# Kernel optimization log

Hardware: AMD Instinct MI355X
Metric: run time of the kernel (lower is better)

## Reference

```python
import jax, jax.numpy as jnp
import numpy as np

NUM_LEVELS = 4
RADIUS = 4


def _avg_pool2(x):
    # x: [N, H, W] -> [N, H//2, W//2], 2x2 mean pool, stride 2 (F.avg_pool2d(corr,2,2))
    N, H, W = x.shape
    return x.reshape(N, H // 2, 2, W // 2, 2).mean(axis=(2, 4))


def _bilinear_sample(img, x, y):
    # img: [N, H, W]; x, y: [N, P] pixel coords.
    # Matches F.grid_sample(..., mode='bilinear', align_corners=True, padding_mode='zeros')
    # after the pixel->normalized->pixel round trip in bilinear_sampler (identity).
    N, H, W = img.shape
    x0 = jnp.floor(x)
    y0 = jnp.floor(y)
    wx = x - x0
    wy = y - y0
    x0i = x0.astype(jnp.int32)
    y0i = y0.astype(jnp.int32)
    flat = img.reshape(N, H * W)

    def gather(yi, xi):
        valid = (xi >= 0) & (xi <= W - 1) & (yi >= 0) & (yi <= H - 1)
        idx = jnp.clip(yi, 0, H - 1) * W + jnp.clip(xi, 0, W - 1)
        v = jnp.take_along_axis(flat, idx, axis=1)
        return jnp.where(valid, v, jnp.zeros((), img.dtype))

    v00 = gather(y0i, x0i)
    v01 = gather(y0i, x0i + 1)
    v10 = gather(y0i + 1, x0i)
    v11 = gather(y0i + 1, x0i + 1)
    return (v00 * (1 - wy) * (1 - wx) + v01 * (1 - wy) * wx
            + v10 * wy * (1 - wx) + v11 * wy * wx)


def _corr_block(fmap1, fmap2, coords):
    B, D, H, W = fmap1.shape
    # all-pairs correlation: [B, H*W, H*W] / sqrt(D)
    f1 = fmap1.reshape(B, D, H * W)
    f2 = fmap2.reshape(B, D, H * W)
    corr = jnp.einsum('bdn,bdm->bnm', f1, f2) / jnp.sqrt(jnp.asarray(D, fmap1.dtype))
    corr = corr.reshape(B * H * W, H, W)
    pyramid = [corr]
    for _ in range(NUM_LEVELS - 1):
        corr = _avg_pool2(corr)
        pyramid.append(corr)

    # coords: [B, 2, H, W] (x, y) -> [B*H*W, 2]
    c = coords.transpose(0, 2, 3, 1).reshape(B * H * W, 2)
    r = RADIUS
    d = jnp.linspace(-r, r, 2 * r + 1)
    dyg, dxg = jnp.meshgrid(d, d, indexing='ij')
    # faithful to torch: delta = stack(meshgrid(dy, dx), -1); channel 0 added to x, 1 to y
    delta = jnp.stack([dyg, dxg], axis=-1).reshape(-1, 2)  # [81, 2]

    outs = []
    for i, lvl in enumerate(pyramid):
        cl = c[:, None, :] / (2.0 ** i) + delta[None, :, :]  # [N, 81, 2]
        s = _bilinear_sample(lvl, cl[..., 0], cl[..., 1])    # [N, 81]
        outs.append(s.reshape(B, H, W, (2 * r + 1) ** 2))
    out = jnp.concatenate(outs, axis=-1)                     # [B, H, W, 4*81]
    return out.transpose(0, 3, 1, 2).astype(jnp.float32)


def setup_inputs() -> dict:
    key = jax.random.key(0)
    k1, k2, k3 = jax.random.split(key, 3)
    B, D, H, W = 2, 256, 80, 80
    fmap1 = jax.random.normal(k1, (B, D, H, W), dtype=jnp.float32)
    fmap2 = jax.random.normal(k2, (B, D, H, W), dtype=jnp.float32)
    # pixel coords in [0, W-1] x [0, H-1] (channel 0 = x, channel 1 = y)
    u = jax.random.uniform(k3, (B, 2, H, W), dtype=jnp.float32)
    scale = jnp.asarray([W - 1, H - 1], jnp.float32).reshape(1, 2, 1, 1)
    coords = u * scale
    return {"fmap1": fmap1, "fmap2": fmap2, "coords": coords}


def reference(fmap1, fmap2, coords):
    return _corr_block(fmap1, fmap2, coords)
```

## Files before the change

kernel.cpp:

```cpp
#include <hip/hip_runtime.h>


typedef _Float16 h2 __attribute__((ext_vector_type(2)));
typedef _Float16 half8 __attribute__((ext_vector_type(8)));
typedef float f32x4 __attribute__((ext_vector_type(4)));

#define HWDIM 80
#define DCH 256
#define NPIX 12800
#define NBUCKET 800

__global__ __launch_bounds__(256) void transpose_all(const float* __restrict__ f1,
                                                     const float* __restrict__ f2,
                                                     _Float16* __restrict__ f1h,
                                                     _Float16* __restrict__ f2p0) {
    __shared__ float tile[256][33];
    int bid = blockIdx.x;
    bool isf1 = bid < 400;
    int lb = isf1 ? bid : bid - 400;
    const float* src = isf1 ? f1 : f2;
    int b = lb / 200;
    int s0 = (lb % 200) * 32;
    int t = threadIdx.x;
    const float* sb = src + (size_t)b * DCH * (HWDIM * HWDIM);
#pragma unroll 4
    for (int k = 0; k < 32; ++k) {
        int j = t + 256 * k;
        int c = j >> 5, s = j & 31;
        tile[c][s] = sb[(size_t)c * (HWDIM * HWDIM) + s0 + s];
    }
    __syncthreads();
    int p = t & 127;
    int srow = t >> 7;
    if (isf1) {
        _Float16* db = f1h + ((size_t)b * 6400 + s0) * DCH;
#pragma unroll 4
        for (int k = 0; k < 16; ++k) {
            int s = 2 * k + srow;
            h2 v;
            v[0] = (_Float16)tile[2 * p][s];
            v[1] = (_Float16)tile[2 * p + 1][s];
            *(h2*)(db + (size_t)s * DCH + 2 * p) = v;
        }
    } else {
#pragma unroll 4
        for (int k = 0; k < 16; ++k) {
            int s = 2 * k + srow;
            int spatial = s0 + s;
            int yy = spatial / 80;
            int xx = spatial - yy * 80;
            h2 v;
            v[0] = (_Float16)tile[2 * p][s];
            v[1] = (_Float16)tile[2 * p + 1][s];
            size_t off = (size_t)b * 2073600 + (size_t)(p >> 4) * 259200
                       + ((size_t)(yy + 5) * 90 + (xx + 5)) * 32 + ((2 * p) & 31);
            *(h2*)(f2p0 + off) = v;
        }
    }
}

__global__ __launch_bounds__(256) void pool1(const _Float16* __restrict__ src,
                                             _Float16* __restrict__ dst) {
    int i = blockIdx.x * 256 + threadIdx.x;
    int c2 = i & 15;
    int r = i >> 4;
    int x = r % 40; r /= 40;
    int y = r % 40; r /= 40;
    int pl = r & 7;
    int b = r >> 3;
    const h2* s = (const h2*)src + ((size_t)b * 2073600 + (size_t)pl * 259200) / 2
                + ((size_t)(2 * y + 5) * 90 + (2 * x + 5)) * 16 + c2;
    h2 v00 = s[0], v01 = s[16], v10 = s[90 * 16], v11 = s[90 * 16 + 16];
    float r0 = ((float)v00[0] + (float)v01[0] + (float)v10[0] + (float)v11[0]) * 0.25f;
    float r1 = ((float)v00[1] + (float)v01[1] + (float)v10[1] + (float)v11[1]) * 0.25f;
    h2 o; o[0] = (_Float16)r0; o[1] = (_Float16)r1;
    *((h2*)dst + ((size_t)b * 640000 + (size_t)pl * 80000) / 2
      + ((size_t)(y + 5) * 50 + (x + 5)) * 16 + c2) = o;
}

__global__ __launch_bounds__(256) void pool23(const _Float16* __restrict__ l1,
                                              _Float16* __restrict__ l2,
                                              _Float16* __restrict__ l3) {
    int i = blockIdx.x * 256 + threadIdx.x;
    if (i < 102400) {
        int c2 = i & 15;
        int r = i >> 4;
        int x = r % 20; r /= 20;
        int y = r % 20; r /= 20;
        int pl = r & 7;
        int b = r >> 3;
        const h2* s = (const h2*)l1 + ((size_t)b * 640000 + (size_t)pl * 80000) / 2
                    + ((size_t)(2 * y + 5) * 50 + (2 * x + 5)) * 16 + c2;
        h2 v00 = s[0], v01 = s[16], v10 = s[50 * 16], v11 = s[50 * 16 + 16];
        float r0 = ((float)v00[0] + (float)v01[0] + (float)v10[0] + (float)v11[0]) * 0.25f;
        float r1 = ((float)v00[1] + (float)v01[1] + (float)v10[1] + (float)v11[1]) * 0.25f;
        h2 o; o[0] = (_Float16)r0; o[1] = (_Float16)r1;
        *((h2*)l2 + ((size_t)b * 230400 + (size_t)pl * 28800) / 2
          + ((size_t)(y + 5) * 30 + (x + 5)) * 16 + c2) = o;
    } else {
        int j = i - 102400;
        int c2 = j & 15;
        int r = j >> 4;
        int x = r % 10; r /= 10;
        int y = r % 10; r /= 10;
        int pl = r & 7;
        int b = r >> 3;
        const h2* s = (const h2*)l1 + ((size_t)b * 640000 + (size_t)pl * 80000) / 2 + c2;
        float r0 = 0.f, r1 = 0.f;
#pragma unroll
        for (int dy = 0; dy < 4; ++dy)
#pragma unroll
            for (int dx = 0; dx < 4; ++dx) {
                h2 v = s[((size_t)(4 * y + dy + 5) * 50 + (4 * x + dx + 5)) * 16];
                r0 += (float)v[0];
                r1 += (float)v[1];
            }
        h2 o; o[0] = (_Float16)(r0 * 0.0625f); o[1] = (_Float16)(r1 * 0.0625f);
        *((h2*)l3 + ((size_t)b * 102400 + (size_t)pl * 12800) / 2
          + ((size_t)(y + 5) * 20 + (x + 5)) * 16 + c2) = o;
    }
}

static __device__ __forceinline__ int bucket_of(const float* coords, int n) {
    int b = n / 6400;
    int r = n - b * 6400;
    float cx = coords[(size_t)b * 12800 + r];
    float cy = coords[(size_t)b * 12800 + 6400 + r];
    int ix = min(max((int)floorf(cx), 0), 79);
    int iy = min(max((int)floorf(cy), 0), 79);
    return b * 400 + (iy >> 2) * 20 + (ix >> 2);
}

__global__ __launch_bounds__(1024) void bucket_k(const float* __restrict__ coords,
                                                 int* __restrict__ sortedIdxP,
                                                 int* __restrict__ rank) {
    __shared__ unsigned int histS[NBUCKET], scanS[1024], startS[NBUCKET], curS[NBUCKET];
    int t = threadIdx.x;
    if (t < NBUCKET) histS[t] = 0u;
    __syncthreads();
    int bkt[13];
#pragma unroll
    for (int i = 0; i < 13; ++i) {
        int n = i * 1024 + t;
        if (n < NPIX) {
            bkt[i] = bucket_of(coords, n);
            atomicAdd(&histS[bkt[i]], 1u);
        }
    }
    __syncthreads();
    scanS[t] = (t < NBUCKET) ? ((histS[t] + 15u) & ~15u) : 0u;
    __syncthreads();
    for (int d = 1; d < 1024; d <<= 1) {
        unsigned int v = (t >= d) ? scanS[t - d] : 0u;
        __syncthreads();
        scanS[t] += v;
        __syncthreads();
    }
    if (t < NBUCKET) {
        unsigned int e = t ? scanS[t - 1] : 0u;
        startS[t] = e;
        curS[t] = e;
    }
    __syncthreads();
#pragma unroll
    for (int i = 0; i < 13; ++i) {
        int n = i * 1024 + t;
        if (n < NPIX) {
            unsigned int pos = atomicAdd(&curS[bkt[i]], 1u);
            sortedIdxP[pos] = n;
            rank[n] = (int)pos;
        }
    }
    __syncthreads();
    if (t < NBUCKET) {
        unsigned int h = histS[t];
        if (h) {
            unsigned int pc = (h + 15u) & ~15u;
            unsigned int base = startS[t];
            int dup = sortedIdxP[base];
            for (unsigned int s = h; s < pc; ++s) sortedIdxP[base + s] = dup;
        }
    }
}

__global__ __launch_bounds__(512) void corr_mfma(
    const _Float16* __restrict__ f1h,
    const _Float16* __restrict__ f2p0, const _Float16* __restrict__ f2p1,
    const _Float16* __restrict__ f2p2, const _Float16* __restrict__ f2p3,
    const float* __restrict__ coords, const int* __restrict__ sortedIdxP,
    _Float16* __restrict__ scratch) {
    __shared__ float G[176 * 17];
    __shared__ float fxS[4][16], fyS[4][16];
    __shared__ int lxS[4][16], lyS[4][16];
    __shared__ int X0cS[4], Y0cS[4], bS;

    int pphys = blockIdx.x;
    int l = (pphys & 7) * 200 + (pphys >> 3);
    int tid = threadIdx.x;
    if (sortedIdxP[l * 16] < 0) return;
    int lane = tid & 63;
    int wave = tid >> 6;

    int npx = sortedIdxP[l * 16 + (lane & 15)];
    const float4* f1p = (const float4*)(f1h + (size_t)npx * DCH);
    half8 bf[8];
#pragma unroll
    for (int kk = 0; kk < 8; ++kk)
        bf[kk] = __builtin_bit_cast(half8, f1p[(lane >> 4) + 4 * kk]);

    if (tid < 64) {
        int px = tid & 15, Lt = tid >> 4;
        int n = sortedIdxP[l * 16 + px];
        int b = n / 6400;
        int r = n - b * 6400;
        float cx = coords[(size_t)b * 12800 + r];
        float cy = coords[(size_t)b * 12800 + 6400 + r];
        float ls = 1.0f / (float)(1 << Lt);
        float cxl = cx * ls, cyl = cy * ls;
        float fxf = floorf(cxl), fyf = floorf(cyl);
        int X0 = (int)fxf - 4, Y0 = (int)fyf - 4;
        int ix = min(max((int)floorf(cx), 0), 79);
        int iy = min(max((int)floorf(cy), 0), 79);
        int X0c = (((ix >> 2) * 4) >> Lt) - 4;
        int Y0c = (((iy >> 2) * 4) >> Lt) - 4;
        lxS[Lt][px] = min(max(X0 - X0c, 0), 3);
        lyS[Lt][px] = min(max(Y0 - Y0c, 0), 3);
        fxS[Lt][px] = cxl - fxf;
        fyS[Lt][px] = cyl - fyf;
        X0cS[Lt] = X0c;
        Y0cS[Lt] = Y0c;
        if (tid == 0) bS = sortedIdxP[l * 16] / 6400;
    }
    __syncthreads();
    int b = bS;
    _Float16* sc = scratch + (size_t)l * 5184;

    const int WwT[4]  = {13, 11, 10, 10};
    const int MT[4]   = {169, 121, 100, 100};
    const int NTT[4]  = {11, 8, 7, 7};
    const int MAGT[4] = {161320, 190652, 209716, 209716};
    const int WpT[4]  = {90, 50, 30, 20};
    const int PST[4]  = {259200, 80000, 28800, 12800};
    const int PBT[4]  = {2073600, 640000, 230400, 102400};

#pragma unroll
    for (int L = 0; L < 4; ++L) {
        const _Float16* f2L = (L == 0 ? f2p0 : L == 1 ? f2p1 : L == 2 ? f2p2 : f2p3);
        const int Ww = WwT[L], Wp = WpT[L];
        const _Float16* f2b = f2L + (size_t)b * PBT[L]
                            + ((size_t)(Y0cS[L] + 5) * Wp + (X0cS[L] + 5)) * 32;
        for (int rt = wave; rt < NTT[L]; rt += 8) {
            int m = min(rt * 16 + (lane & 15), MT[L] - 1);
            int my = (m * MAGT[L]) >> 21;
            int mx = m - my * Ww;
            const float4* ap = (const float4*)(f2b + (size_t)(my * Wp + mx) * 32)
                             + (lane >> 4);
            f32x4 acc = {0.f, 0.f, 0.f, 0.f};
#pragma unroll
            for (int kk = 0; kk < 8; ++kk) {
                half8 av = __builtin_bit_cast(half8, ap[kk * (PST[L] / 8)]);
                acc = __builtin_amdgcn_mfma_f32_16x16x32_f16(av, bf[kk], acc, 0, 0, 0);
            }
            int gr = rt * 16 + (lane >> 4) * 4;
#pragma unroll
            for (int r = 0; r < 4; ++r) G[(gr + r) * 17 + (lane & 15)] = acc[r];
        }
        __syncthreads();
        for (int idx = tid; idx < 1296; idx += 512) {
            int k = idx >> 4, x = idx & 15;
            int a = (k * 57) >> 9;
            int c = k - 9 * a;
            int gx = lxS[L][x] + a, gy = lyS[L][x] + c;
            int m00 = gy * Ww + gx;
            float fx = fxS[L][x], fy = fyS[L][x];
            float t00 = G[m00 * 17 + x];
            float t01 = G[(m00 + 1) * 17 + x];
            float t10 = G[(m00 + Ww) * 17 + x];
            float t11 = G[(m00 + Ww + 1) * 17 + x];
            float v = ((1.f - fy) * ((1.f - fx) * t00 + fx * t01)
                     + fy * ((1.f - fx) * t10 + fx * t11)) * 0.0625f;
            sc[L * 1296 + k * 16 + x] = (_Float16)v;
        }
        __syncthreads();
    }
}

__global__ __launch_bounds__(256) void unsort4(const _Float16* __restrict__ scratch,
                                               const int* __restrict__ rank,
                                               float* __restrict__ out) {
    int u = blockIdx.x * 256 + threadIdx.x;
    int q = u % 1600;
    int ch = (u / 1600) % 324;
    int b = u / (1600 * 324);
    int nl = q * 4;
    int4 rk = *(const int4*)(rank + b * 6400 + nl);
    float4 v;
    v.x = (float)scratch[(size_t)(rk.x >> 4) * 5184 + ch * 16 + (rk.x & 15)];
    v.y = (float)scratch[(size_t)(rk.y >> 4) * 5184 + ch * 16 + (rk.y & 15)];
    v.z = (float)scratch[(size_t)(rk.z >> 4) * 5184 + ch * 16 + (rk.z & 15)];
    v.w = (float)scratch[(size_t)(rk.w >> 4) * 5184 + ch * 16 + (rk.w & 15)];
    *(float4*)(out + ((size_t)b * 324 + ch) * 6400 + nl) = v;
}

extern "C" void kernel_launch(void* const* d_in, const int* in_sizes, int n_in,
                              void* d_out, int out_size, void* d_ws, size_t ws_size,
                              hipStream_t stream) {
    const float* fmap1 = (const float*)d_in[0];
    const float* fmap2 = (const float*)d_in[1];
    const float* coords = (const float*)d_in[2];
    float* out = (float*)d_out;
    char* ws = (char*)d_ws;

    _Float16* f1h  = (_Float16*)(ws);
    _Float16* f2p0 = (_Float16*)(ws + 6553600);
    _Float16* f2p1 = (_Float16*)(ws + 14848000);
    _Float16* f2p2 = (_Float16*)(ws + 17408000);
    _Float16* f2p3 = (_Float16*)(ws + 18329600);
    int* sortedIdxP = (int*)(ws + 18739200);
    int* rank       = (int*)(ws + 18841600);
    _Float16* scratch = (_Float16*)(ws + 18892800);

    hipMemsetAsync(f2p0, 0, 12185600, stream);
    hipMemsetAsync(sortedIdxP, 0xFF, 102400, stream);

    transpose_all<<<dim3(800), dim3(256), 0, stream>>>(fmap1, fmap2, f1h, f2p0);
    pool1<<<dim3(1600), dim3(256), 0, stream>>>(f2p0, f2p1);
    pool23<<<dim3(500), dim3(256), 0, stream>>>(f2p1, f2p2, f2p3);
    bucket_k<<<dim3(1), dim3(1024), 0, stream>>>(coords, sortedIdxP, rank);
    corr_mfma<<<dim3(1600), dim3(512), 0, stream>>>(f1h, f2p0, f2p1, f2p2, f2p3,
                                                    coords, sortedIdxP, scratch);
    unsort4<<<dim3(4050), dim3(256), 0, stream>>>(scratch, rank, out);
}
```

Before: 106.3 us.

## Merge per-level MFMA tiles into one pass, replace bucket scan with wave shuffles

The correlation kernel now computes all 33 MFMA row tiles for the four pyramid levels in a single flattened loop, spread round-robin over the 8 waves, into a larger shared G buffer. Bilinear interpolation for all levels then runs in one pass. This drops the seven per-level block barriers and the poor wave utilisation on the levels that have fewer tiles than waves. The cost is more shared memory per block, which may lower occupancy, and a launch-bounds hint of 4 that could limit registers. Separately, the bucket kernel's 10-step barrier-based block scan is replaced by a wave-shuffle scan followed by a scan over the per-wave sums.

```diff
diff --git a/kernel.cpp b/kernel.cpp
--- a/kernel.cpp
+++ b/kernel.cpp
@@ -134,7 +134,8 @@
 __global__ __launch_bounds__(1024) void bucket_k(const float* __restrict__ coords,
                                                  int* __restrict__ sortedIdxP,
                                                  int* __restrict__ rank) {
-    __shared__ unsigned int histS[NBUCKET], scanS[1024], startS[NBUCKET], curS[NBUCKET];
+    __shared__ unsigned int histS[NBUCKET], startS[NBUCKET], curS[NBUCKET];
+    __shared__ unsigned int waveSum[16];
     int t = threadIdx.x;
     if (t < NBUCKET) histS[t] = 0u;
     __syncthreads();
@@ -148,16 +149,28 @@
         }
     }
     __syncthreads();
-    scanS[t] = (t < NBUCKET) ? ((histS[t] + 15u) & ~15u) : 0u;
-    __syncthreads();
-    for (int d = 1; d < 1024; d <<= 1) {
-        unsigned int v = (t >= d) ? scanS[t - d] : 0u;
-        __syncthreads();
-        scanS[t] += v;
-        __syncthreads();
-    }
+    unsigned int v = (t < NBUCKET) ? ((histS[t] + 15u) & ~15u) : 0u;
+    unsigned int x = v;
+#pragma unroll
+    for (int d = 1; d < 64; d <<= 1) {
+        unsigned int y = __shfl_up(x, d);
+        if ((t & 63) >= d) x += y;
+    }
+    if ((t & 63) == 63) waveSum[t >> 6] = x;
+    __syncthreads();
+    if (t < 16) {
+        unsigned int w = waveSum[t];
+#pragma unroll
+        for (int d = 1; d < 16; d <<= 1) {
+            unsigned int y = __shfl_up(w, d);
+            if (t >= d) w += y;
+        }
+        waveSum[t] = w;
+    }
+    __syncthreads();
+    unsigned int incl = x + ((t >> 6) ? waveSum[(t >> 6) - 1] : 0u);
     if (t < NBUCKET) {
-        unsigned int e = t ? scanS[t - 1] : 0u;
+        unsigned int e = incl - v;
         startS[t] = e;
         curS[t] = e;
     }
@@ -183,13 +196,13 @@
     }
 }
 
-__global__ __launch_bounds__(512) void corr_mfma(
+__global__ __launch_bounds__(512, 4) void corr_mfma(
     const _Float16* __restrict__ f1h,
     const _Float16* __restrict__ f2p0, const _Float16* __restrict__ f2p1,
     const _Float16* __restrict__ f2p2, const _Float16* __restrict__ f2p3,
     const float* __restrict__ coords, const int* __restrict__ sortedIdxP,
     _Float16* __restrict__ scratch) {
-    __shared__ float G[176 * 17];
+    __shared__ float G[528 * 17];
     __shared__ float fxS[4][16], fyS[4][16];
     __shared__ int lxS[4][16], lyS[4][16];
     __shared__ int X0cS[4], Y0cS[4], bS;
@@ -235,53 +248,56 @@
     int b = bS;
     _Float16* sc = scratch + (size_t)l * 5184;
 
-    const int WwT[4]  = {13, 11, 10, 10};
-    const int MT[4]   = {169, 121, 100, 100};
-    const int NTT[4]  = {11, 8, 7, 7};
-    const int MAGT[4] = {161320, 190652, 209716, 209716};
-    const int WpT[4]  = {90, 50, 30, 20};
-    const int PST[4]  = {259200, 80000, 28800, 12800};
-    const int PBT[4]  = {2073600, 640000, 230400, 102400};
-
-#pragma unroll
-    for (int L = 0; L < 4; ++L) {
+#pragma unroll
+    for (int tt = 0; tt < 33; ++tt) {
+        const int L  = tt < 11 ? 0 : tt < 19 ? 1 : tt < 26 ? 2 : 3;
+        const int rt = tt - (L == 0 ? 0 : L == 1 ? 11 : L == 2 ? 19 : 26);
+        const int Ww = L == 0 ? 13 : L == 1 ? 11 : 10;
+        const int MT = L == 0 ? 169 : L == 1 ? 121 : 100;
+        const int MAG = L == 0 ? 161320 : L == 1 ? 190652 : 209716;
+        const int Wp = L == 0 ? 90 : L == 1 ? 50 : L == 2 ? 30 : 20;
+        const int PS = L == 0 ? 259200 : L == 1 ? 80000 : L == 2 ? 28800 : 12800;
+        const int PB = L == 0 ? 2073600 : L == 1 ? 640000 : L == 2 ? 230400 : 102400;
+        const int GO = L == 0 ? 0 : L == 1 ? 176 : L == 2 ? 304 : 416;
+        if (tt == 32 ? (wave != 7) : ((tt & 7) != wave)) continue;
         const _Float16* f2L = (L == 0 ? f2p0 : L == 1 ? f2p1 : L == 2 ? f2p2 : f2p3);
-        const int Ww = WwT[L], Wp = WpT[L];
-        const _Float16* f2b = f2L + (size_t)b * PBT[L]
+        const _Float16* f2b = f2L + (size_t)b * PB
                             + ((size_t)(Y0cS[L] + 5) * Wp + (X0cS[L] + 5)) * 32;
-        for (int rt = wave; rt < NTT[L]; rt += 8) {
-            int m = min(rt * 16 + (lane & 15), MT[L] - 1);
-            int my = (m * MAGT[L]) >> 21;
-            int mx = m - my * Ww;
-            const float4* ap = (const float4*)(f2b + (size_t)(my * Wp + mx) * 32)
-                             + (lane >> 4);
-            f32x4 acc = {0.f, 0.f, 0.f, 0.f};
-#pragma unroll
-            for (int kk = 0; kk < 8; ++kk) {
-                half8 av = __builtin_bit_cast(half8, ap[kk * (PST[L] / 8)]);
-                acc = __builtin_amdgcn_mfma_f32_16x16x32_f16(av, bf[kk], acc, 0, 0, 0);
-            }
-            int gr = rt * 16 + (lane >> 4) * 4;
-#pragma unroll
-            for (int r = 0; r < 4; ++r) G[(gr + r) * 17 + (lane & 15)] = acc[r];
-        }
-        __syncthreads();
-        for (int idx = tid; idx < 1296; idx += 512) {
-            int k = idx >> 4, x = idx & 15;
-            int a = (k * 57) >> 9;
-            int c = k - 9 * a;
-            int gx = lxS[L][x] + a, gy = lyS[L][x] + c;
-            int m00 = gy * Ww + gx;
-            float fx = fxS[L][x], fy = fyS[L][x];
-            float t00 = G[m00 * 17 + x];
-            float t01 = G[(m00 + 1) * 17 + x];
-            float t10 = G[(m00 + Ww) * 17 + x];
-            float t11 = G[(m00 + Ww + 1) * 17 + x];
-            float v = ((1.f - fy) * ((1.f - fx) * t00 + fx * t01)
-                     + fy * ((1.f - fx) * t10 + fx * t11)) * 0.0625f;
-            sc[L * 1296 + k * 16 + x] = (_Float16)v;
-        }
-        __syncthreads();
+        int m = min(rt * 16 + (lane & 15), MT - 1);
+        int my = (m * MAG) >> 21;
+        int mx = m - my * Ww;
+        const float4* ap = (const float4*)(f2b + (size_t)(my * Wp + mx) * 32)
+                         + (lane >> 4);
+        f32x4 acc = {0.f, 0.f, 0.f, 0.f};
+#pragma unroll
+        for (int kk = 0; kk < 8; ++kk) {
+            half8 av = __builtin_bit_cast(half8, ap[kk * (PS / 8)]);
+            acc = __builtin_amdgcn_mfma_f32_16x16x32_f16(av, bf[kk], acc, 0, 0, 0);
+        }
+        int gr = GO + rt * 16 + (lane >> 4) * 4;
+#pragma unroll
+        for (int r = 0; r < 4; ++r) G[(gr + r) * 17 + (lane & 15)] = acc[r];
+    }
+    __syncthreads();
+
+    for (int idx = tid; idx < 5184; idx += 512) {
+        int k2 = idx >> 4, x = idx & 15;
+        int Le = (k2 * 810) >> 16;
+        int k = k2 - Le * 81;
+        int Ww = Le == 0 ? 13 : Le == 1 ? 11 : 10;
+        int GO = Le == 0 ? 0 : Le == 1 ? 176 : Le == 2 ? 304 : 416;
+        int a = (k * 57) >> 9;
+        int c = k - 9 * a;
+        int gx = lxS[Le][x] + a, gy = lyS[Le][x] + c;
+        int m00 = GO + gy * Ww + gx;
+        float fx = fxS[Le][x], fy = fyS[Le][x];
+        float t00 = G[m00 * 17 + x];
+        float t01 = G[(m00 + 1) * 17 + x];
+        float t10 = G[(m00 + Ww) * 17 + x];
+        float t11 = G[(m00 + Ww + 1) * 17 + x];
+        float v = ((1.f - fy) * ((1.f - fx) * t00 + fx * t01)
+                 + fy * ((1.f - fx) * t10 + fx * t11)) * 0.0625f;
+        sc[idx] = (_Float16)v;
     }
 }
 
```

After: 104.3 us. About the same (-1.8%).
